# Optimization experiments

Measured on AMD Instinct MI355X. Metric: run time of the kernel, lower is better.

## Reference

```python
import jax, jax.numpy as jnp
import numpy as np

D_MODEL = 1024
NUM_HEADS = 16
HEAD_DIM = D_MODEL // NUM_HEADS


def setup_inputs() -> dict:
    key = jax.random.key(0)
    ks = jax.random.split(key, 9)
    s = 0.02
    return {
        "x": jax.random.normal(ks[0], (4, 2048, D_MODEL), dtype=jnp.float32),
        "Wq": jax.random.normal(ks[1], (D_MODEL, D_MODEL), dtype=jnp.float32) * s,
        "bq": jnp.zeros((D_MODEL,), dtype=jnp.float32),
        "Wk": jax.random.normal(ks[2], (D_MODEL, D_MODEL), dtype=jnp.float32) * s,
        "bk": jnp.zeros((D_MODEL,), dtype=jnp.float32),
        "Wv": jax.random.normal(ks[3], (D_MODEL, D_MODEL), dtype=jnp.float32) * s,
        "bv": jnp.zeros((D_MODEL,), dtype=jnp.float32),
        "Wo": jax.random.normal(ks[4], (D_MODEL, D_MODEL), dtype=jnp.float32) * s,
        "bo": jnp.zeros((D_MODEL,), dtype=jnp.float32),
    }


def reference(x, Wq, bq, Wk, bk, Wv, bv, Wo, bo):
    B, S, D = x.shape
    H, Hd = NUM_HEADS, HEAD_DIM

    def split_heads(t):  # [B,S,D] -> [B,H,S,Hd]
        return t.reshape(B, S, H, Hd).transpose(0, 2, 1, 3)

    q = split_heads(x @ Wq + bq)
    k = split_heads(x @ Wk + bk)
    v = split_heads(x @ Wv + bv)

    scale = 1.0 / jnp.sqrt(jnp.float32(Hd))
    scores = jnp.einsum("bhqd,bhkd->bhqk", q, k) * scale  # [B,H,S,S]
    attn = jax.nn.softmax(scores, axis=-1)
    # dropout(p=0.1) is identity in eval mode
    ctx = jnp.einsum("bhqk,bhkd->bhqd", attn, v)
    ctx = ctx.transpose(0, 2, 1, 3).reshape(B, S, D)
    return ctx @ Wo + bo
```

## Files before the change

### kernel.cpp

```cpp
#include <hip/hip_runtime.h>
#include <hip/hip_bf16.h>

typedef __bf16 bf16;
typedef bf16 bf16x8 __attribute__((ext_vector_type(8)));
typedef bf16 bf16x4v __attribute__((ext_vector_type(4)));
typedef bf16 bf16x2v __attribute__((ext_vector_type(2)));
typedef float f32x4 __attribute__((ext_vector_type(4)));
typedef float f32x16 __attribute__((ext_vector_type(16)));
typedef unsigned int uint;
typedef uint uint4v __attribute__((ext_vector_type(4)));

#define D_MODEL 1024
#define SEQ     2048
#define BATCH   4
#define NHEAD   16
#define HDIM    64
#define MTOK    8192
#define RSZ     ((size_t)MTOK * D_MODEL)
#define QSCALE  0.18033688011112042f

#define GLD16(src, dst)                                                        \
  __builtin_amdgcn_global_load_lds(                                            \
      (const __attribute__((address_space(1))) void*)(src),                    \
      (__attribute__((address_space(3))) void*)(dst), 16, 0, 0)

#define WAITVM(N) asm volatile("s_waitcnt vmcnt(" #N ")" ::: "memory")
#define BAR() __builtin_amdgcn_s_barrier()
#define SCHEDBAR() __builtin_amdgcn_sched_barrier(0)

#define PSWAP(a, b) asm("v_permlane32_swap_b32 %0, %1" : "+v"(a), "+v"(b))

#define MFMA16(a, b, c) __builtin_amdgcn_mfma_f32_16x16x32_bf16((a), (b), (c), 0, 0, 0)

__device__ __forceinline__ uint pk2(float lo, float hi) {
  bf16x2v h;
  h[0] = (bf16)lo;
  h[1] = (bf16)hi;
  return __builtin_bit_cast(uint, h);
}

__global__ __launch_bounds__(256) void cvt_x_kernel(const float* __restrict__ x,
                                                    bf16* __restrict__ xb) {
  int i = blockIdx.x * 256 + threadIdx.x;
  f32x4 v = ((const f32x4*)x)[i];
  bf16x4v o;
#pragma unroll
  for (int c = 0; c < 4; ++c) o[c] = (bf16)v[c];
  ((bf16x4v*)xb)[i] = o;
}

__global__ __launch_bounds__(256) void wtrans_kernel(
    const float* __restrict__ Wq, const float* __restrict__ Wk,
    const float* __restrict__ Wv, const float* __restrict__ Wo,
    bf16* __restrict__ wt, bf16* __restrict__ wot) {
  __shared__ float t[32][33];
  int z = blockIdx.z;
  const float* W = (z == 0) ? Wq : (z == 1) ? Wk : (z == 2) ? Wv : Wo;
  bf16* dst = (z < 3) ? (wt + (size_t)z * D_MODEL * D_MODEL) : wot;
  int tx = threadIdx.x, ty = threadIdx.y;
  int bx = blockIdx.x * 32, by = blockIdx.y * 32;
#pragma unroll
  for (int j = 0; j < 4; ++j)
    t[ty + j * 8][tx] = W[(size_t)(by + ty + j * 8) * D_MODEL + bx + tx];
  __syncthreads();
#pragma unroll
  for (int j = 0; j < 4; ++j)
    dst[(size_t)(bx + ty + j * 8) * D_MODEL + by + tx] = (bf16)t[tx][ty + j * 8];
}

__global__ __launch_bounds__(256) void vtrans_kernel(const bf16* __restrict__ V,
                                                     bf16* __restrict__ Vt) {
  __shared__ bf16 Ls[128][72];
  const int st = blockIdx.x, bh = blockIdx.y;
  const bf16* src = V + ((size_t)bh * SEQ + st * 128) * HDIM;
  bf16* dst = Vt + (size_t)bh * HDIM * SEQ + st * 128;
  const int t = threadIdx.x;
  const int r = t >> 3, d0 = (t & 7) * 8;
#pragma unroll
  for (int j = 0; j < 4; ++j)
    *(bf16x8*)&Ls[r + j * 32][d0] = *(const bf16x8*)(src + (size_t)(r + j * 32) * HDIM + d0);
  __syncthreads();
  const int d = t & 63, sc = (t >> 6) * 32;
#pragma unroll
  for (int c = 0; c < 4; ++c) {
    bf16x8 v;
#pragma unroll
    for (int i = 0; i < 8; ++i) v[i] = Ls[sc + c * 8 + i][d];
    *(bf16x8*)(dst + (size_t)d * SEQ + sc + c * 8) = v;
  }
}

__global__ __launch_bounds__(512, 2) void gemm256(
    const bf16* __restrict__ A, const bf16* __restrict__ Bt,
    const float* __restrict__ bias0, const float* __restrict__ bias1,
    const float* __restrict__ bias2, bf16* __restrict__ qkvb) {
  __shared__ __align__(16) char lds[131072];
  const int tid = threadIdx.x;
  const int w = tid >> 6, lane = tid & 63;
  const int l15 = lane & 15, l16 = lane >> 4;
  const int NX = 12;
  const int bx = blockIdx.x % NX, by = blockIdx.x / NX;
  const int rowBase = by * 256, colBase = bx * 256;

  const int srow0 = tid >> 3, srow1 = (512 + tid) >> 3;
  const int sch0 = (tid & 7) ^ (srow0 & 7);
  const int sch1 = (tid & 7) ^ (srow1 & 7);
  const bf16* gA = A + (size_t)rowBase * 1024;
  const bf16* gB = Bt + (size_t)colBase * 1024;
  const int wb0 = (tid & ~63) * 16;
  const int wb1 = (512 + (tid & ~63)) * 16;

#define STG_A(b, h, kt)                                                                   \
  do {                                                                                    \
    GLD16(gA + (size_t)((h)*128 + srow0) * 1024 + (kt)*64 + sch0 * 8,                     \
          lds + (b)*32768 + (h)*16384 + wb0);                                             \
    GLD16(gA + (size_t)((h)*128 + srow1) * 1024 + (kt)*64 + sch1 * 8,                     \
          lds + (b)*32768 + (h)*16384 + wb1);                                             \
  } while (0)
#define STG_B(b, h, kt)                                                                   \
  do {                                                                                    \
    GLD16(gB + (size_t)((h)*128 + srow0) * 1024 + (kt)*64 + sch0 * 8,                     \
          lds + 65536 + (b)*32768 + (h)*16384 + wb0);                                     \
    GLD16(gB + (size_t)((h)*128 + srow1) * 1024 + (kt)*64 + sch1 * 8,                     \
          lds + 65536 + (b)*32768 + (h)*16384 + wb1);                                     \
  } while (0)

  const int arow = (w & 3) * 32 + l15;
  const int brow = (w >> 2) * 64 + l15;
  int achk[2];
#pragma unroll
  for (int ks = 0; ks < 2; ++ks) achk[ks] = ((ks * 4 + l16) ^ (l15 & 7)) * 16;
#define AOFF(qm, mi, ks) (((qm)*128 + arow + (mi)*16) * 128 + achk[ks])
#define BOFF(qn, ni, ks) (((qn)*128 + brow + (ni)*16) * 128 + achk[ks])

  f32x4 acc[2][2][2][4] = {};

  STG_A(0, 0, 0);
  STG_B(0, 0, 0);
  STG_A(0, 1, 0);
  STG_B(0, 1, 0);

#define TILE_BODY(T, SON, W0, W1, W2)                                                     \
  {                                                                                       \
    const int cb = (T)&1, nb = cb ^ 1;                                                    \
    const char* At = lds + cb * 32768;                                                    \
    const char* Bl = lds + 65536 + cb * 32768;                                            \
    WAITVM(W0);                                                                           \
    BAR();                                                                                \
    if (SON) STG_A(nb, 0, (T) + 1);                                                       \
    bf16x8 a0f[2][2], b0f[4][2];                                                          \
    _Pragma("unroll") for (int mi = 0; mi < 2; ++mi)                                      \
        _Pragma("unroll") for (int ks = 0; ks < 2; ++ks)                                  \
            a0f[mi][ks] = *(const bf16x8*)(At + AOFF(0, mi, ks));                         \
    _Pragma("unroll") for (int ni = 0; ni < 4; ++ni)                                      \
        _Pragma("unroll") for (int ks = 0; ks < 2; ++ks)                                  \
            b0f[ni][ks] = *(const bf16x8*)(Bl + BOFF(0, ni, ks));                         \
    __builtin_amdgcn_s_setprio(1);                                                        \
    _Pragma("unroll") for (int mi = 0; mi < 2; ++mi)                                      \
        _Pragma("unroll") for (int ni = 0; ni < 4; ++ni) {                                \
      acc[0][0][mi][ni] = MFMA16(a0f[mi][0], b0f[ni][0], acc[0][0][mi][ni]);              \
      acc[0][0][mi][ni] = MFMA16(a0f[mi][1], b0f[ni][1], acc[0][0][mi][ni]);              \
    }                                                                                     \
    __builtin_amdgcn_s_setprio(0);                                                        \
    SCHEDBAR();                                                                           \
    WAITVM(W1);                                                                           \
    BAR();                                                                                \
    if (SON) STG_B(nb, 0, (T) + 1);                                                       \
    bf16x8 a1f[2][2];                                                                     \
    _Pragma("unroll") for (int mi = 0; mi < 2; ++mi)                                      \
        _Pragma("unroll") for (int ks = 0; ks < 2; ++ks)                                  \
            a1f[mi][ks] = *(const bf16x8*)(At + AOFF(1, mi, ks));                         \
    __builtin_amdgcn_s_setprio(1);                                                        \
    _Pragma("unroll") for (int mi = 0; mi < 2; ++mi)                                      \
        _Pragma("unroll") for (int ni = 0; ni < 4; ++ni) {                                \
      acc[1][0][mi][ni] = MFMA16(a1f[mi][0], b0f[ni][0], acc[1][0][mi][ni]);              \
      acc[1][0][mi][ni] = MFMA16(a1f[mi][1], b0f[ni][1], acc[1][0][mi][ni]);              \
    }                                                                                     \
    __builtin_amdgcn_s_setprio(0);                                                        \
    SCHEDBAR();                                                                           \
    WAITVM(W2);                                                                           \
    BAR();                                                                                \
    if (SON) STG_A(nb, 1, (T) + 1);                                                       \
    bf16x8 b1f[4][2];                                                                     \
    _Pragma("unroll") for (int ni = 0; ni < 4; ++ni)                                      \
        _Pragma("unroll") for (int ks = 0; ks < 2; ++ks)                                  \
            b1f[ni][ks] = *(const bf16x8*)(Bl + BOFF(1, ni, ks));                         \
    __builtin_amdgcn_s_setprio(1);                                                        \
    _Pragma("unroll") for (int mi = 0; mi < 2; ++mi)                                      \
        _Pragma("unroll") for (int ni = 0; ni < 4; ++ni) {                                \
      acc[1][1][mi][ni] = MFMA16(a1f[mi][0], b1f[ni][0], acc[1][1][mi][ni]);              \
      acc[1][1][mi][ni] = MFMA16(a1f[mi][1], b1f[ni][1], acc[1][1][mi][ni]);              \
    }                                                                                     \
    __builtin_amdgcn_s_setprio(0);                                                        \
    SCHEDBAR();                                                                           \
    if (SON) STG_B(nb, 1, (T) + 1);                                                       \
    bf16x8 a0g[2][2];                                                                     \
    _Pragma("unroll") for (int mi = 0; mi < 2; ++mi)                                      \
        _Pragma("unroll") for (int ks = 0; ks < 2; ++ks)                                  \
            a0g[mi][ks] = *(const bf16x8*)(At + AOFF(0, mi, ks));                         \
    __builtin_amdgcn_s_setprio(1);                                                        \
    _Pragma("unroll") for (int mi = 0; mi < 2; ++mi)                                      \
        _Pragma("unroll") for (int ni = 0; ni < 4; ++ni) {                                \
      acc[0][1][mi][ni] = MFMA16(a0g[mi][0], b1f[ni][0], acc[0][1][mi][ni]);              \
      acc[0][1][mi][ni] = MFMA16(a0g[mi][1], b1f[ni][1], acc[0][1][mi][ni]);              \
    }                                                                                     \
    __builtin_amdgcn_s_setprio(0);                                                        \
    SCHEDBAR();                                                                           \
  }

  for (int t = 0; t < 15; ++t) TILE_BODY(t, 1, 4, 4, 4);
  TILE_BODY(15, 0, 4, 2, 0);
#undef TILE_BODY
#undef STG_A
#undef STG_B
#undef AOFF
#undef BOFF

  const int rl = l16 * 4;
  const int mat = colBase >> 10;
  const float* bp = (mat == 0) ? bias0 : (mat == 1) ? bias1 : bias2;
  const float scl = (mat == 0) ? QSCALE : 1.0f;
  bf16* dst = qkvb + (size_t)mat * RSZ;
#pragma unroll
  for (int qm = 0; qm < 2; ++qm)
#pragma unroll
    for (int mi = 0; mi < 2; ++mi) {
      int rbase = rowBase + qm * 128 + (w & 3) * 32 + mi * 16 + rl;
#pragma unroll
      for (int qn = 0; qn < 2; ++qn)
#pragma unroll
        for (int ni = 0; ni < 4; ++ni) {
          int n = colBase + qn * 128 + (w >> 2) * 64 + ni * 16 + l15;
          int nn = n & 1023;
          int hh = nn >> 6, dd = nn & 63;
          float bvv = bp[nn];
#pragma unroll
          for (int r = 0; r < 4; ++r) {
            int m = rbase + r;
            int bb2 = m >> 11, ss = m & 2047;
            dst[((size_t)(bb2 * NHEAD + hh) * SEQ + ss) * HDIM + dd] =
                (bf16)((acc[qm][qn][mi][ni][r] + bvv) * scl);
          }
        }
    }
}

__global__ __launch_bounds__(256) void gemm_out(
    const bf16* __restrict__ A, const bf16* __restrict__ Bt,
    const float* __restrict__ bias, float* __restrict__ dst) {
  __shared__ bf16 As[128 * 32];
  __shared__ bf16 Bs[128 * 32];
  const int tid = threadIdx.x;
  const int wave = tid >> 6, lane = tid & 63;
  const int rowBase = blockIdx.y * 128;
  const int colBase = blockIdx.x * 128;
  const int wR = (wave >> 1) * 64;
  const int wC = (wave & 1) * 64;

  const int r0 = tid >> 2, c0 = tid & 3;
  const int cp0 = c0 ^ ((r0 >> 1) & 3);
  const int r1 = 64 + r0;
  const int cp1 = c0 ^ ((r1 >> 1) & 3);
  const bf16* srcA0 = A + (size_t)(rowBase + r0) * 1024 + cp0 * 8;
  const bf16* srcA1 = A + (size_t)(rowBase + r1) * 1024 + cp1 * 8;
  const bf16* srcB0 = Bt + (size_t)(colBase + r0) * 1024 + cp0 * 8;
  const bf16* srcB1 = Bt + (size_t)(colBase + r1) * 1024 + cp1 * 8;
  char* AsB = (char*)As;
  char* BsB = (char*)Bs;
  char* ldsA0 = AsB + wave * 1024;
  char* ldsA1 = AsB + 4096 + wave * 1024;
  char* ldsB0 = BsB + wave * 1024;
  char* ldsB1 = BsB + 4096 + wave * 1024;

  int aoff[4], boff[4];
#pragma unroll
  for (int i = 0; i < 4; ++i) {
    int ra = wR + i * 16 + (lane & 15);
    aoff[i] = ra * 64 + (((lane >> 4) ^ ((ra >> 1) & 3)) * 16);
    int rb = wC + i * 16 + (lane & 15);
    boff[i] = rb * 64 + (((lane >> 4) ^ ((rb >> 1) & 3)) * 16);
  }

  f32x4 acc[4][4] = {};
  for (int k0 = 0; k0 < 1024; k0 += 32) {
    GLD16(srcA0 + k0, ldsA0);
    GLD16(srcA1 + k0, ldsA1);
    GLD16(srcB0 + k0, ldsB0);
    GLD16(srcB1 + k0, ldsB1);
    __syncthreads();
    bf16x8 af[4], bf_[4];
#pragma unroll
    for (int i = 0; i < 4; ++i) af[i] = *(const bf16x8*)(AsB + aoff[i]);
#pragma unroll
    for (int i = 0; i < 4; ++i) bf_[i] = *(const bf16x8*)(BsB + boff[i]);
#pragma unroll
    for (int mi = 0; mi < 4; ++mi)
#pragma unroll
      for (int ni = 0; ni < 4; ++ni)
        acc[mi][ni] = MFMA16(af[mi], bf_[ni], acc[mi][ni]);
    __syncthreads();
  }

  const int rl = (lane >> 4) * 4;
  const int cl = lane & 15;
#pragma unroll
  for (int mi = 0; mi < 4; ++mi) {
    int rbase = rowBase + wR + mi * 16 + rl;
#pragma unroll
    for (int ni = 0; ni < 4; ++ni) {
      int col = colBase + wC + ni * 16 + cl;
      float bvv = bias[col];
#pragma unroll
      for (int r = 0; r < 4; ++r)
        dst[(size_t)(rbase + r) * 1024 + col] = acc[mi][ni][r] + bvv;
    }
  }
}

__global__ __launch_bounds__(256, 3) void attn_kernel(const bf16* __restrict__ qkv,
                                                      const bf16* __restrict__ vt,
                                                      bf16* __restrict__ ctx) {
  __shared__ __align__(16) char smem[32768];
  char* Kbuf = smem;
  char* Vbuf = smem + 16384;

  const int tid = threadIdx.x;
  const int wave = tid >> 6, lane = tid & 63;
  const int l31 = lane & 31, l5 = lane >> 5;
  const int swz = (blockIdx.x & 7) * 128 + (blockIdx.x >> 3);
  const int qt = swz & 15, hh = (swz >> 4) & 15, bb = swz >> 8;
  const int bh = bb * NHEAD + hh;
  const bf16* Qp = qkv + (size_t)bh * SEQ * HDIM;
  const bf16* Kp = qkv + RSZ + (size_t)bh * SEQ * HDIM;
  const bf16* Vtp = vt + (size_t)bh * HDIM * SEQ;

  const int qrow = qt * 128 + wave * 32 + l31;
  bf16x8 qf[4];
#pragma unroll
  for (int kc = 0; kc < 4; ++kc)
    qf[kc] = *(const bf16x8*)(Qp + (size_t)qrow * 64 + kc * 16 + l5 * 8);

  const int sr = tid >> 3;
  const int sz = (tid & 7) ^ (sr & 7);
  const bf16* srcK0 = Kp + sr * 64 + sz * 8;
  const bf16* srcK1 = Kp + (sr + 32) * 64 + sz * 8;
  const bf16* srcV0 = Vtp + (size_t)sr * SEQ + sz * 8;
  const bf16* srcV1 = Vtp + (size_t)(sr + 32) * SEQ + sz * 8;

#define STAGE(sel, t)                                                     \
  do {                                                                    \
    GLD16(srcK0 + (t) * 4096, Kbuf + (sel) * 8192 + wave * 1024);         \
    GLD16(srcK1 + (t) * 4096, Kbuf + (sel) * 8192 + 4096 + wave * 1024);  \
    GLD16(srcV0 + (t) * 64, Vbuf + (sel) * 8192 + wave * 1024);           \
    GLD16(srcV1 + (t) * 64, Vbuf + (sel) * 8192 + 4096 + wave * 1024);    \
  } while (0)

  f32x16 o[2];
#pragma unroll
  for (int nd = 0; nd < 2; ++nd)
#pragma unroll
    for (int r = 0; r < 16; ++r) o[nd][r] = 0.f;
  float l_run = 0.f;

  STAGE(0, 0);

  for (int kt = 0; kt < 32; ++kt) {
    const int cur = kt & 1;
    if (kt < 31) {
      STAGE(cur ^ 1, kt + 1);
      WAITVM(4);
    } else {
      WAITVM(0);
    }
    BAR();

    const char* Kc = Kbuf + cur * 8192;
    const char* Vc = Vbuf + cur * 8192;

    f32x16 s[2];
#pragma unroll
    for (int nb = 0; nb < 2; ++nb)
#pragma unroll
      for (int r = 0; r < 16; ++r) s[nb][r] = 0.f;
    __builtin_amdgcn_s_setprio(1);
#pragma unroll
    for (int nb = 0; nb < 2; ++nb)
#pragma unroll
      for (int kc = 0; kc < 4; ++kc) {
        int row = nb * 32 + l31;
        int off = row * 128 + (((2 * kc + l5) ^ (row & 7)) * 16);
        bf16x8 kf = *(const bf16x8*)(Kc + off);
        s[nb] = __builtin_amdgcn_mfma_f32_32x32x16_bf16(kf, qf[kc], s[nb], 0, 0, 0);
      }
    __builtin_amdgcn_s_setprio(0);

#pragma unroll
    for (int nb = 0; nb < 2; ++nb)
#pragma unroll
      for (int r = 0; r < 16; ++r)
        s[nb][r] = __builtin_amdgcn_exp2f(s[nb][r]);

    f32x16 tv = s[0] + s[1];
    float q8[8];
#pragma unroll
    for (int r = 0; r < 8; ++r) q8[r] = tv[r] + tv[r + 8];
#pragma unroll
    for (int r = 0; r < 4; ++r) q8[r] += q8[r + 4];
    float rs = (q8[0] + q8[1]) + (q8[2] + q8[3]);
    rs += __shfl_xor(rs, 32, 64);
    l_run += rs;

    bf16x8 pf[4];
#pragma unroll
    for (int cc = 0; cc < 4; ++cc) {
      const int nb = cc >> 1, b0 = (cc & 1) * 8;
      uint w0 = pk2(s[nb][b0 + 0], s[nb][b0 + 1]);
      uint w1 = pk2(s[nb][b0 + 2], s[nb][b0 + 3]);
      uint w2 = pk2(s[nb][b0 + 4], s[nb][b0 + 5]);
      uint w3 = pk2(s[nb][b0 + 6], s[nb][b0 + 7]);
      PSWAP(w0, w2);
      PSWAP(w1, w3);
      uint4v u = {w0, w1, w2, w3};
      pf[cc] = __builtin_bit_cast(bf16x8, u);
    }

    __builtin_amdgcn_s_setprio(1);
#pragma unroll
    for (int nd = 0; nd < 2; ++nd)
#pragma unroll
      for (int cc = 0; cc < 4; ++cc) {
        int row = nd * 32 + l31;
        int off = row * 128 + (((2 * cc + l5) ^ (row & 7)) * 16);
        bf16x8 vf = *(const bf16x8*)(Vc + off);
        o[nd] = __builtin_amdgcn_mfma_f32_32x32x16_bf16(vf, pf[cc], o[nd], 0, 0, 0);
      }
    __builtin_amdgcn_s_setprio(0);
    BAR();
  }

  const float inv = 1.0f / l_run;
  bf16* crow = ctx + (size_t)(bb * SEQ + qrow) * D_MODEL + hh * HDIM;
#pragma unroll
  for (int nd = 0; nd < 2; ++nd)
#pragma unroll
    for (int a = 0; a < 4; ++a) {
      bf16x4v p4;
#pragma unroll
      for (int b = 0; b < 4; ++b) p4[b] = (bf16)(o[nd][4 * a + b] * inv);
      *(bf16x4v*)(crow + nd * 32 + a * 8 + l5 * 4) = p4;
    }
#undef STAGE
}

extern "C" void kernel_launch(void* const* d_in, const int* in_sizes, int n_in,
                              void* d_out, int out_size, void* d_ws, size_t ws_size,
                              hipStream_t stream) {
  const float* x  = (const float*)d_in[0];
  const float* Wq = (const float*)d_in[1];
  const float* bq = (const float*)d_in[2];
  const float* Wk = (const float*)d_in[3];
  const float* bk = (const float*)d_in[4];
  const float* Wv = (const float*)d_in[5];
  const float* bv = (const float*)d_in[6];
  const float* Wo = (const float*)d_in[7];
  const float* bo = (const float*)d_in[8];

  char* ws = (char*)d_ws;
  bf16* xb   = (bf16*)(ws);
  bf16* vtb  = (bf16*)(ws);
  bf16* wt   = (bf16*)(ws + (size_t)16 * 1024 * 1024);
  bf16* wot  = (bf16*)(ws + (size_t)22 * 1024 * 1024);
  bf16* qkvb = (bf16*)(ws + (size_t)24 * 1024 * 1024);
  bf16* ctxb = (bf16*)(ws + (size_t)72 * 1024 * 1024);

  cvt_x_kernel<<<8192, 256, 0, stream>>>(x, xb);
  wtrans_kernel<<<dim3(32, 32, 4), dim3(32, 8), 0, stream>>>(Wq, Wk, Wv, Wo, wt, wot);
  gemm256<<<384, 512, 0, stream>>>(xb, wt, bq, bk, bv, qkvb);
  vtrans_kernel<<<dim3(16, 64), 256, 0, stream>>>(qkvb + 2 * RSZ, vtb);
  attn_kernel<<<1024, 256, 0, stream>>>(qkvb, vtb, ctxb);
  gemm_out<<<dim3(8, 64), 256, 0, stream>>>(ctxb, wot, bo, (float*)d_out);
}
```

Measured before the change: 289.5 us.

## Software-pipeline attention loop: overlap QK of next tile with PV of previous

Restructures the attention inner loop so the QK^T MFMAs and softmax for tile kt run in the same iteration as the PV MFMAs for tile kt-1. This lets the exp and pack work interleave with matrix ops instead of serialising them. V gets a triple buffer (LDS grows from 32KB to 40KB), and the loop now waits for all loads once per iteration with a single barrier. The cost is more LDS and live registers (two P fragment sets), which may hurt occupancy at 3 blocks/CU, and the full vmcnt(0) wait removes some prefetch slack.

```diff
diff --git a/kernel.cpp b/kernel.cpp
--- a/kernel.cpp
+++ b/kernel.cpp
@@ -320,7 +320,7 @@
 __global__ __launch_bounds__(256, 3) void attn_kernel(const bf16* __restrict__ qkv,
                                                       const bf16* __restrict__ vt,
                                                       bf16* __restrict__ ctx) {
-  __shared__ __align__(16) char smem[32768];
+  __shared__ __align__(16) char smem[40960];
   char* Kbuf = smem;
   char* Vbuf = smem + 16384;
 
@@ -347,12 +347,72 @@
   const bf16* srcV0 = Vtp + (size_t)sr * SEQ + sz * 8;
   const bf16* srcV1 = Vtp + (size_t)(sr + 32) * SEQ + sz * 8;
 
-#define STAGE(sel, t)                                                     \
+#define STAGE_K(koff, t)                                                  \
   do {                                                                    \
-    GLD16(srcK0 + (t) * 4096, Kbuf + (sel) * 8192 + wave * 1024);         \
-    GLD16(srcK1 + (t) * 4096, Kbuf + (sel) * 8192 + 4096 + wave * 1024);  \
-    GLD16(srcV0 + (t) * 64, Vbuf + (sel) * 8192 + wave * 1024);           \
-    GLD16(srcV1 + (t) * 64, Vbuf + (sel) * 8192 + 4096 + wave * 1024);    \
+    GLD16(srcK0 + (t) * 4096, Kbuf + (koff) + wave * 1024);               \
+    GLD16(srcK1 + (t) * 4096, Kbuf + (koff) + 4096 + wave * 1024);        \
+  } while (0)
+#define STAGE_V(voff, t)                                                  \
+  do {                                                                    \
+    GLD16(srcV0 + (t) * 64, Vbuf + (voff) + wave * 1024);                 \
+    GLD16(srcV1 + (t) * 64, Vbuf + (voff) + 4096 + wave * 1024);          \
+  } while (0)
+
+#define QK_BLOCK(koff)                                                    \
+  do {                                                                    \
+    const char* Kc = Kbuf + (koff);                                       \
+    _Pragma("unroll") for (int nb = 0; nb < 2; ++nb)                      \
+        _Pragma("unroll") for (int r = 0; r < 16; ++r) s[nb][r] = 0.f;    \
+    __builtin_amdgcn_s_setprio(1);                                        \
+    _Pragma("unroll") for (int nb = 0; nb < 2; ++nb)                      \
+        _Pragma("unroll") for (int kc = 0; kc < 4; ++kc) {                \
+      int row = nb * 32 + l31;                                            \
+      int off = row * 128 + (((2 * kc + l5) ^ (row & 7)) * 16);           \
+      bf16x8 kf = *(const bf16x8*)(Kc + off);                             \
+      s[nb] = __builtin_amdgcn_mfma_f32_32x32x16_bf16(kf, qf[kc], s[nb],  \
+                                                      0, 0, 0);           \
+    }                                                                     \
+    __builtin_amdgcn_s_setprio(0);                                        \
+  } while (0)
+
+#define SM_PACK(pf)                                                       \
+  do {                                                                    \
+    _Pragma("unroll") for (int nb = 0; nb < 2; ++nb)                      \
+        _Pragma("unroll") for (int r = 0; r < 16; ++r)                    \
+            s[nb][r] = __builtin_amdgcn_exp2f(s[nb][r]);                  \
+    f32x16 tv = s[0] + s[1];                                              \
+    float q8[8];                                                          \
+    _Pragma("unroll") for (int r = 0; r < 8; ++r) q8[r] = tv[r] + tv[r + 8]; \
+    _Pragma("unroll") for (int r = 0; r < 4; ++r) q8[r] += q8[r + 4];     \
+    float rs = (q8[0] + q8[1]) + (q8[2] + q8[3]);                         \
+    rs += __shfl_xor(rs, 32, 64);                                         \
+    l_run += rs;                                                          \
+    _Pragma("unroll") for (int cc = 0; cc < 4; ++cc) {                    \
+      const int nb = cc >> 1, b0 = (cc & 1) * 8;                          \
+      uint w0 = pk2(s[nb][b0 + 0], s[nb][b0 + 1]);                        \
+      uint w1 = pk2(s[nb][b0 + 2], s[nb][b0 + 3]);                        \
+      uint w2 = pk2(s[nb][b0 + 4], s[nb][b0 + 5]);                        \
+      uint w3 = pk2(s[nb][b0 + 6], s[nb][b0 + 7]);                        \
+      PSWAP(w0, w2);                                                      \
+      PSWAP(w1, w3);                                                      \
+      uint4v u = {w0, w1, w2, w3};                                        \
+      pf[cc] = __builtin_bit_cast(bf16x8, u);                             \
+    }                                                                     \
+  } while (0)
+
+#define PV_BLOCK(pf, voff)                                                \
+  do {                                                                    \
+    const char* Vc = Vbuf + (voff);                                       \
+    __builtin_amdgcn_s_setprio(1);                                        \
+    _Pragma("unroll") for (int nd = 0; nd < 2; ++nd)                      \
+        _Pragma("unroll") for (int cc = 0; cc < 4; ++cc) {                \
+      int row = nd * 32 + l31;                                            \
+      int off = row * 128 + (((2 * cc + l5) ^ (row & 7)) * 16);           \
+      bf16x8 vf = *(const bf16x8*)(Vc + off);                             \
+      o[nd] = __builtin_amdgcn_mfma_f32_32x32x16_bf16(vf, pf[cc], o[nd],  \
+                                                      0, 0, 0);           \
+    }                                                                     \
+    __builtin_amdgcn_s_setprio(0);                                        \
   } while (0)
 
   f32x16 o[2];
@@ -361,82 +421,39 @@
 #pragma unroll
     for (int r = 0; r < 16; ++r) o[nd][r] = 0.f;
   float l_run = 0.f;
-
-  STAGE(0, 0);
-
-  for (int kt = 0; kt < 32; ++kt) {
-    const int cur = kt & 1;
+  f32x16 s[2];
+  bf16x8 pfp[4];
+
+  STAGE_K(0, 0);
+  STAGE_V(0, 0);
+
+  WAITVM(0);
+  BAR();
+  STAGE_K(8192, 1);
+  STAGE_V(8192, 1);
+  QK_BLOCK(0);
+  SM_PACK(pfp);
+
+  int pvs = 0, cvs = 8192, nvs = 16384;
+  for (int kt = 1; kt < 32; ++kt) {
+    WAITVM(0);
+    BAR();
     if (kt < 31) {
-      STAGE(cur ^ 1, kt + 1);
-      WAITVM(4);
-    } else {
-      WAITVM(0);
+      STAGE_K(((kt + 1) & 1) * 8192, kt + 1);
+      STAGE_V(nvs, kt + 1);
     }
-    BAR();
-
-    const char* Kc = Kbuf + cur * 8192;
-    const char* Vc = Vbuf + cur * 8192;
-
-    f32x16 s[2];
-#pragma unroll
-    for (int nb = 0; nb < 2; ++nb)
-#pragma unroll
-      for (int r = 0; r < 16; ++r) s[nb][r] = 0.f;
-    __builtin_amdgcn_s_setprio(1);
-#pragma unroll
-    for (int nb = 0; nb < 2; ++nb)
-#pragma unroll
-      for (int kc = 0; kc < 4; ++kc) {
-        int row = nb * 32 + l31;
-        int off = row * 128 + (((2 * kc + l5) ^ (row & 7)) * 16);
-        bf16x8 kf = *(const bf16x8*)(Kc + off);
-        s[nb] = __builtin_amdgcn_mfma_f32_32x32x16_bf16(kf, qf[kc], s[nb], 0, 0, 0);
-      }
-    __builtin_amdgcn_s_setprio(0);
-
-#pragma unroll
-    for (int nb = 0; nb < 2; ++nb)
-#pragma unroll
-      for (int r = 0; r < 16; ++r)
-        s[nb][r] = __builtin_amdgcn_exp2f(s[nb][r]);
-
-    f32x16 tv = s[0] + s[1];
-    float q8[8];
-#pragma unroll
-    for (int r = 0; r < 8; ++r) q8[r] = tv[r] + tv[r + 8];
-#pragma unroll
-    for (int r = 0; r < 4; ++r) q8[r] += q8[r + 4];
-    float rs = (q8[0] + q8[1]) + (q8[2] + q8[3]);
-    rs += __shfl_xor(rs, 32, 64);
-    l_run += rs;
-
-    bf16x8 pf[4];
-#pragma unroll
-    for (int cc = 0; cc < 4; ++cc) {
-      const int nb = cc >> 1, b0 = (cc & 1) * 8;
-      uint w0 = pk2(s[nb][b0 + 0], s[nb][b0 + 1]);
-      uint w1 = pk2(s[nb][b0 + 2], s[nb][b0 + 3]);
-      uint w2 = pk2(s[nb][b0 + 4], s[nb][b0 + 5]);
-      uint w3 = pk2(s[nb][b0 + 6], s[nb][b0 + 7]);
-      PSWAP(w0, w2);
-      PSWAP(w1, w3);
-      uint4v u = {w0, w1, w2, w3};
-      pf[cc] = __builtin_bit_cast(bf16x8, u);
-    }
-
-    __builtin_amdgcn_s_setprio(1);
-#pragma unroll
-    for (int nd = 0; nd < 2; ++nd)
-#pragma unroll
-      for (int cc = 0; cc < 4; ++cc) {
-        int row = nd * 32 + l31;
-        int off = row * 128 + (((2 * cc + l5) ^ (row & 7)) * 16);
-        bf16x8 vf = *(const bf16x8*)(Vc + off);
-        o[nd] = __builtin_amdgcn_mfma_f32_32x32x16_bf16(vf, pf[cc], o[nd], 0, 0, 0);
-      }
-    __builtin_amdgcn_s_setprio(0);
-    BAR();
+    QK_BLOCK((kt & 1) * 8192);
+    bf16x8 pfc[4];
+    SM_PACK(pfc);
+    PV_BLOCK(pfp, pvs);
+#pragma unroll
+    for (int cc = 0; cc < 4; ++cc) pfp[cc] = pfc[cc];
+    int tmp = pvs;
+    pvs = cvs;
+    cvs = nvs;
+    nvs = tmp;
   }
+  PV_BLOCK(pfp, pvs);
 
   const float inv = 1.0f / l_run;
   bf16* crow = ctx + (size_t)(bb * SEQ + qrow) * D_MODEL + hh * HDIM;
@@ -449,7 +466,11 @@
       for (int b = 0; b < 4; ++b) p4[b] = (bf16)(o[nd][4 * a + b] * inv);
       *(bf16x4v*)(crow + nd * 32 + a * 8 + l5 * 4) = p4;
     }
-#undef STAGE
+#undef STAGE_K
+#undef STAGE_V
+#undef QK_BLOCK
+#undef SM_PACK
+#undef PV_BLOCK
 }
 
 extern "C" void kernel_launch(void* const* d_in, const int* in_sizes, int n_in,
```

Result: faster. 282.8 us (-2.3%).

## Fuse V transpose into QKV GEMM epilogue via LDS-staged vectorized stores

Applied to the files above, without the earlier changes.

The QKV GEMM epilogue now stages each 128-row half of the output tile in LDS, then writes Q and K with 16-byte vector stores in head-split layout. V is written directly in transposed [bh, d, s] layout. This removes the separate vtrans kernel launch and its extra round trip of V through global memory, and replaces the scattered 2-byte stores. The cost is two extra barriers and LDS traffic in the epilogue, plus column-strided LDS reads for the V transpose that may hit bank conflicts.

```diff
diff --git a/kernel.cpp b/kernel.cpp
--- a/kernel.cpp
+++ b/kernel.cpp
@@ -66,28 +66,6 @@
 #pragma unroll
   for (int j = 0; j < 4; ++j)
     dst[(size_t)(bx + ty + j * 8) * D_MODEL + by + tx] = (bf16)t[tx][ty + j * 8];
-}
-
-__global__ __launch_bounds__(256) void vtrans_kernel(const bf16* __restrict__ V,
-                                                     bf16* __restrict__ Vt) {
-  __shared__ bf16 Ls[128][72];
-  const int st = blockIdx.x, bh = blockIdx.y;
-  const bf16* src = V + ((size_t)bh * SEQ + st * 128) * HDIM;
-  bf16* dst = Vt + (size_t)bh * HDIM * SEQ + st * 128;
-  const int t = threadIdx.x;
-  const int r = t >> 3, d0 = (t & 7) * 8;
-#pragma unroll
-  for (int j = 0; j < 4; ++j)
-    *(bf16x8*)&Ls[r + j * 32][d0] = *(const bf16x8*)(src + (size_t)(r + j * 32) * HDIM + d0);
-  __syncthreads();
-  const int d = t & 63, sc = (t >> 6) * 32;
-#pragma unroll
-  for (int c = 0; c < 4; ++c) {
-    bf16x8 v;
-#pragma unroll
-    for (int i = 0; i < 8; ++i) v[i] = Ls[sc + c * 8 + i][d];
-    *(bf16x8*)(dst + (size_t)d * SEQ + sc + c * 8) = v;
-  }
 }
 
 __global__ __launch_bounds__(512, 2) void gemm256(
@@ -220,29 +198,55 @@
   const int mat = colBase >> 10;
   const float* bp = (mat == 0) ? bias0 : (mat == 1) ? bias1 : bias2;
   const float scl = (mat == 0) ? QSCALE : 1.0f;
-  bf16* dst = qkvb + (size_t)mat * RSZ;
-#pragma unroll
-  for (int qm = 0; qm < 2; ++qm)
-#pragma unroll
-    for (int mi = 0; mi < 2; ++mi) {
-      int rbase = rowBase + qm * 128 + (w & 3) * 32 + mi * 16 + rl;
-#pragma unroll
-      for (int qn = 0; qn < 2; ++qn)
+  const int LDT = 264;
+  bf16* T = (bf16*)lds;
+  const int bb2 = rowBase >> 11;
+  const int hh0 = (colBase & 1023) >> 6;
+  const int cloc = colBase & 1023;
+
+  for (int qm = 0; qm < 2; ++qm) {
+    BAR();
+#pragma unroll
+    for (int qn = 0; qn < 2; ++qn)
+#pragma unroll
+      for (int mi = 0; mi < 2; ++mi)
 #pragma unroll
         for (int ni = 0; ni < 4; ++ni) {
-          int n = colBase + qn * 128 + (w >> 2) * 64 + ni * 16 + l15;
-          int nn = n & 1023;
-          int hh = nn >> 6, dd = nn & 63;
-          float bvv = bp[nn];
-#pragma unroll
-          for (int r = 0; r < 4; ++r) {
-            int m = rbase + r;
-            int bb2 = m >> 11, ss = m & 2047;
-            dst[((size_t)(bb2 * NHEAD + hh) * SEQ + ss) * HDIM + dd] =
-                (bf16)((acc[qm][qn][mi][ni][r] + bvv) * scl);
-          }
+          int c = qn * 128 + (w >> 2) * 64 + ni * 16 + l15;
+          float bvv = bp[cloc + c];
+          int s0 = (w & 3) * 32 + mi * 16 + rl;
+#pragma unroll
+          for (int r = 0; r < 4; ++r)
+            T[(s0 + r) * LDT + c] = (bf16)((acc[qm][qn][mi][ni][r] + bvv) * scl);
         }
+    BAR();
+    const int ssBase = (rowBase & 2047) + qm * 128;
+    if (mat < 2) {
+      bf16* dst = qkvb + (size_t)mat * RSZ;
+#pragma unroll
+      for (int j = 0; j < 8; ++j) {
+        int u = j * 512 + tid;
+        int row = u >> 3, ck = u & 7;
+        int hl = row >> 7, s = row & 127;
+        bf16x8 v = *(const bf16x8*)&T[s * LDT + hl * 64 + ck * 8];
+        *(bf16x8*)(dst + ((size_t)(bb2 * NHEAD + hh0 + hl) * SEQ + ssBase + s) * HDIM +
+                   ck * 8) = v;
+      }
+    } else {
+      bf16* vtb = qkvb + 2 * RSZ;
+      int rv = tid >> 1, hf = tid & 1;
+      int hl = rv >> 6, dd = rv & 63;
+      bf16* drow = vtb + ((size_t)(bb2 * NHEAD + hh0 + hl) * HDIM + dd) * SEQ + ssBase +
+                   hf * 64;
+#pragma unroll
+      for (int g = 0; g < 8; ++g) {
+        bf16x8 v;
+#pragma unroll
+        for (int i = 0; i < 8; ++i) v[i] = T[(hf * 64 + g * 8 + i) * LDT + hl * 64 + dd];
+        *(bf16x8*)(drow + g * 8) = v;
+      }
     }
+  }
 }
 
 __global__ __launch_bounds__(256) void gemm_out(
@@ -467,7 +471,6 @@
 
   char* ws = (char*)d_ws;
   bf16* xb   = (bf16*)(ws);
-  bf16* vtb  = (bf16*)(ws);
   bf16* wt   = (bf16*)(ws + (size_t)16 * 1024 * 1024);
   bf16* wot  = (bf16*)(ws + (size_t)22 * 1024 * 1024);
   bf16* qkvb = (bf16*)(ws + (size_t)24 * 1024 * 1024);
@@ -476,7 +479,6 @@
   cvt_x_kernel<<<8192, 256, 0, stream>>>(x, xb);
   wtrans_kernel<<<dim3(32, 32, 4), dim3(32, 8), 0, stream>>>(Wq, Wk, Wv, Wo, wt, wot);
   gemm256<<<384, 512, 0, stream>>>(xb, wt, bq, bk, bv, qkvb);
-  vtrans_kernel<<<dim3(16, 64), 256, 0, stream>>>(qkvb + 2 * RSZ, vtb);
-  attn_kernel<<<1024, 256, 0, stream>>>(qkvb, vtb, ctxb);
+  attn_kernel<<<1024, 256, 0, stream>>>(qkvb, qkvb + 2 * RSZ, ctxb);
   gemm_out<<<dim3(8, 64), 256, 0, stream>>>(ctxb, wot, bo, (float*)d_out);
 }
```

New measurement: 280.2 us. -3.2%, faster.
